# Performance work log

Measured on AMD Instinct MI355X. Metric: run time of the kernel, lower is better.

Reference implementation:

```python
import math
import jax, jax.numpy as jnp
import numpy as np

B, S, E, H = 4, 1024, 768, 12
HD = E // H
NUM_BUCKETS, MAX_DIST = 320, 800


def setup_inputs() -> dict:
    key = jax.random.key(0)
    ks = jax.random.split(key, 8)
    w = lambda k, sh: jax.random.normal(k, sh, jnp.float32) * 0.02
    return {
        "hidden_states": jax.random.normal(ks[0], (B, S, E), jnp.float32),
        "q_w": w(ks[1], (E, E)), "q_b": jnp.zeros((E,), jnp.float32),
        "k_w": w(ks[2], (E, E)), "k_b": jnp.zeros((E,), jnp.float32),
        "v_w": w(ks[3], (E, E)), "v_b": jnp.zeros((E,), jnp.float32),
        "out_w": w(ks[4], (E, E)), "out_b": jnp.zeros((E,), jnp.float32),
        "gru_const": jnp.ones((1, H, 1, 1), jnp.float32),
        "gru_w": w(ks[5], (8, HD)), "gru_b": jnp.zeros((8,), jnp.float32),
        "rel_embed": w(ks[6], (NUM_BUCKETS, H)),
    }


def _relative_positions_bucket(rel):
    # rel: (S, S) int32, rel = memory_pos - context_pos
    nb = NUM_BUCKETS // 2
    buckets = (rel > 0).astype(jnp.int32) * nb
    rel = jnp.abs(rel)
    max_exact = nb // 2
    is_small = rel < max_exact
    large = jnp.log(rel.astype(jnp.float32) / max_exact)
    large = large / math.log(MAX_DIST / max_exact) * (nb - max_exact)
    large = (max_exact + large).astype(jnp.int32)
    large = jnp.minimum(large, nb - 1)
    return buckets + jnp.where(is_small, rel, large)


def _compute_position_bias(rel_embed):
    pos = jnp.arange(S, dtype=jnp.int32)
    rel = pos[None, :] - pos[:, None]              # (S, S)
    bucket = _relative_positions_bucket(rel)       # (S, S) int32
    return rel_embed[bucket].transpose(2, 0, 1)    # (H, S, S)


def reference(hidden_states, q_w, q_b, k_w, k_b, v_w, v_b, out_w, out_b,
              gru_const, gru_w, gru_b, rel_embed):
    position_bias = _compute_position_bias(rel_embed)          # (H, S, S)

    # gated relative-position bias
    ghs = hidden_states.reshape(B, S, H, HD).transpose(0, 2, 1, 3)   # (B,H,S,HD)
    proj = jnp.einsum("bhsd,ed->bhse", ghs, gru_w) + gru_b           # (B,H,S,8)
    proj = proj.reshape(B, H, S, 2, 4).sum(-1)                       # (B,H,S,2)
    gates = jax.nn.sigmoid(proj)
    gate_a, gate_b = gates[..., 0:1], gates[..., 1:2]                # (B,H,S,1)
    gate = gate_a * (gate_b * gru_const - 1.0) + 2.0                 # (B,H,S,1)
    gated_bias = gate[..., None, :, 0][..., None] * 0  # placeholder removed below
    gated_bias = gate * position_bias[None]                          # (B,H,S,S)

    scaling = HD ** -0.5
    q = (hidden_states @ q_w.T + q_b).reshape(B, S, H, HD).transpose(0, 2, 1, 3) * scaling
    k = (hidden_states @ k_w.T + k_b).reshape(B, S, H, HD).transpose(0, 2, 1, 3)
    v = (hidden_states @ v_w.T + v_b).reshape(B, S, H, HD).transpose(0, 2, 1, 3)

    scores = jnp.einsum("bhqd,bhkd->bhqk", q, k) + gated_bias
    attn = jax.nn.softmax(scores, axis=-1)
    ctx = jnp.einsum("bhqk,bhkd->bhqd", attn, v)                     # (B,H,S,HD)
    ctx = ctx.transpose(0, 2, 1, 3).reshape(B, S, E)
    attn_output = ctx @ out_w.T + out_b
    return attn_output, position_bias
```

## Files before the change

### kernel.cpp

```cpp
#include <hip/hip_runtime.h>

typedef unsigned short u16;
typedef __attribute__((ext_vector_type(4))) unsigned short u16x4;
typedef __attribute__((ext_vector_type(8))) short s8v;
typedef __attribute__((ext_vector_type(4))) float f4v;

#define BB 4
#define SS 1024
#define EE 768
#define HH 12
#define DD 64

#define NHS (BB * SS * EE)
#define NW  (EE * EE)
#define LOG2E 1.4426950408889634f

static __device__ __forceinline__ u16 f2bf(float x){
  unsigned int u = __float_as_uint(x);
  u += 0x7fffu + ((u >> 16) & 1u);
  return (u16)(u >> 16);
}
static __device__ __forceinline__ unsigned cvt_pk_bf16(float lo, float hi){
  unsigned r;
  asm("v_cvt_pk_bf16_f32 %0, %1, %2" : "=v"(r) : "v"(lo), "v"(hi));
  return r;
}
static __device__ __forceinline__ void stage16(const u16* g, u16* l){
  __builtin_amdgcn_global_load_lds(
      (const __attribute__((address_space(1))) void*)g,
      (__attribute__((address_space(3))) void*)l, 16, 0, 0);
}

__global__ __launch_bounds__(256) void prep_kernel(const float* __restrict__ hs,
                                                   const float* __restrict__ qw,
                                                   const float* __restrict__ kw,
                                                   const float* __restrict__ vw,
                                                   const float* __restrict__ ow,
                                                   u16* __restrict__ dst,
                                                   const float* __restrict__ rel_embed,
                                                   float* __restrict__ tbl,
                                                   const float* __restrict__ gru_w,
                                                   const float* __restrict__ gru_b,
                                                   const float* __restrict__ gru_c,
                                                   float* __restrict__ gate){
  const int bid = blockIdx.x;
  if (bid < 2688){
    size_t e = ((size_t)bid * 256 + threadIdx.x) * 8;
    const float* src;
    if      (e < (size_t)NHS)            src = hs + e;
    else if (e < (size_t)NHS + NW)       src = qw + (e - NHS);
    else if (e < (size_t)NHS + 2 * NW)   src = kw + (e - NHS - NW);
    else if (e < (size_t)NHS + 3 * NW)   src = vw + (e - NHS - 2 * (size_t)NW);
    else                                 src = ow + (e - NHS - 3 * (size_t)NW);
    f4v v0 = *(const f4v*)src, v1 = *(const f4v*)(src + 4);
    s8v o;
    #pragma unroll
    for (int i = 0; i < 4; i++){ o[i] = (short)f2bf(v0[i]); o[4 + i] = (short)f2bf(v1[i]); }
    size_t row = e / EE;
    int k = (int)(e - row * EE);
    size_t d = row * EE + (size_t)(k ^ (((int)row & 7) << 3));
    *(s8v*)(dst + d) = o;
  } else if (bid < 2784){
    int id = (bid - 2688) * 256 + threadIdx.x;
    int h = id >> 11, r = id & 2047;
    float v = 0.f;
    if (r < 2047){
      int rel = r - 1023;
      int bucket = (rel > 0) ? 160 : 0;
      int a = rel < 0 ? -rel : rel;
      int idx;
      if (a < 80) idx = a;
      else {
        float t = logf((float)a / 80.0f);
        t = t / 2.302585092994046f * 80.0f;
        int lg = (int)(80.0f + t);
        idx = lg < 159 ? lg : 159;
      }
      v = rel_embed[(idx + bucket) * HH + h];
    }
    tbl[id] = v;
  } else {
    int wid = (bid - 2784) * 4 + (threadIdx.x >> 6);
    int lane = threadIdx.x & 63;
    int s = wid & (SS - 1);
    int bh = wid >> 10;
    int h = bh % HH, b = bh / HH;
    float x = hs[(size_t)(b * SS + s) * EE + h * DD + lane];
    float w0 = gru_w[lane] + gru_w[64 + lane] + gru_w[128 + lane] + gru_w[192 + lane];
    float w1 = gru_w[256 + lane] + gru_w[320 + lane] + gru_w[384 + lane] + gru_w[448 + lane];
    float y0 = x * w0, y1 = x * w1;
    #pragma unroll
    for (int off = 1; off < 64; off <<= 1){
      y0 += __shfl_xor(y0, off);
      y1 += __shfl_xor(y1, off);
    }
    if (lane == 0){
      float s0 = y0 + gru_b[0] + gru_b[1] + gru_b[2] + gru_b[3];
      float s1 = y1 + gru_b[4] + gru_b[5] + gru_b[6] + gru_b[7];
      float ga = 1.f / (1.f + __expf(-s0));
      float gb = 1.f / (1.f + __expf(-s1));
      gate[wid] = ga * (gb * gru_c[h] - 1.0f) + 2.0f;
    }
  }
}

template<int EP>
static __device__ __forceinline__ void gemm_body(const u16* __restrict__ A,
                                                 const u16* __restrict__ Bw,
                                                 const float* __restrict__ bias,
                                                 void* __restrict__ Cp,
                                                 float scale, int m0, int n0){
  __shared__ __align__(16) u16 a_s[128 * 64];
  __shared__ __align__(16) u16 b_s[128 * 64];
  const int t = threadIdx.x;
  const int wave = t >> 6, lane = t & 63;
  const int lr = lane & 15, lg = lane >> 4;
  const int wm = (wave >> 1) * 64, wn = (wave & 1) * 64;
  const int srow = lane >> 3;
  const int scol = (lane & 7) * 8;
  const int swz = (lr & 7) << 3;

  const f4v zero = {0.f, 0.f, 0.f, 0.f};
  f4v acc[4][4];
  #pragma unroll
  for (int i = 0; i < 4; i++)
    #pragma unroll
    for (int j = 0; j < 4; j++) acc[i][j] = zero;

  for (int k0 = 0; k0 < EE; k0 += 64){
    if (k0) __syncthreads();
    #pragma unroll
    for (int i = 0; i < 4; i++){
      const int chunk = i * 4 + wave;
      const int r = chunk * 8 + srow;
      stage16(A  + (size_t)(m0 + r) * EE + k0 + scol, &a_s[chunk * 512]);
      stage16(Bw + (size_t)(n0 + r) * EE + k0 + scol, &b_s[chunk * 512]);
    }
    __syncthreads();
    #pragma unroll
    for (int kk = 0; kk < 2; kk++){
      const int cbase = (kk * 32 + lg * 8) ^ swz;
      s8v af[4], bf[4];
      #pragma unroll
      for (int i = 0; i < 4; i++){
        af[i] = *(const s8v*)&a_s[(wm + i * 16 + lr) * 64 + cbase];
        bf[i] = *(const s8v*)&b_s[(wn + i * 16 + lr) * 64 + cbase];
      }
      #pragma unroll
      for (int i = 0; i < 4; i++)
        #pragma unroll
        for (int j = 0; j < 4; j++)
          acc[i][j] = __builtin_amdgcn_mfma_f32_16x16x32_bf16(af[i], bf[j], acc[i][j], 0, 0, 0);
    }
  }

  #pragma unroll
  for (int ii = 0; ii < 4; ii++){
    const int row0 = m0 + wm + ii * 16 + lg * 4;
    const int bb = row0 >> 10;
    const int s0 = row0 & (SS - 1);
    #pragma unroll
    for (int j = 0; j < 4; j++){
      const int col = n0 + wn + j * 16 + lr;
      const float bv = bias[col];
      if (EP == 0){
        const int h = col >> 6, dim = col & 63;
        const int bh = bb * HH + h;
        u16* dst = (u16*)Cp + ((size_t)((bh * 64 + (s0 >> 4)) * 2 + (dim >> 5))) * 512
                   + ((dim >> 3) & 3) * 128 + (s0 & 15) * 8 + (dim & 7);
        #pragma unroll
        for (int r = 0; r < 4; r++)
          dst[r * 8] = f2bf((acc[ii][j][r] + bv) * scale);
      } else if (EP == 2){
        const int h = col >> 6, dim = col & 63;
        const int bh = bb * HH + h;
        u16x4 pk;
        #pragma unroll
        for (int r = 0; r < 4; r++) pk[r] = f2bf(acc[ii][j][r] + bv);
        *(u16x4*)((u16*)Cp + ((size_t)(((bh * 16 + (s0 >> 6)) * 2 + ((s0 >> 5) & 1)) * 4 + (dim >> 4))) * 512
                  + ((s0 >> 3) & 3) * 128 + (dim & 15) * 8 + (s0 & 7)) = pk;
      } else {
        #pragma unroll
        for (int r = 0; r < 4; r++)
          ((float*)Cp)[(size_t)(row0 + r) * EE + col] = acc[ii][j][r] + bv;
      }
    }
  }
}

__global__ __launch_bounds__(256) void gemm_qkv(const u16* __restrict__ A,
                                                const u16* __restrict__ wqkv,
                                                const float* __restrict__ bq,
                                                const float* __restrict__ bk,
                                                const float* __restrict__ bv,
                                                u16* __restrict__ qo,
                                                u16* __restrict__ ko,
                                                u16* __restrict__ vo){
  const int z = blockIdx.z;
  if (z == 2)
    gemm_body<2>(A, wqkv + 2 * (size_t)NW, bv, vo, 1.0f, blockIdx.x * 128, blockIdx.y * 128);
  else
    gemm_body<0>(A, wqkv + (size_t)z * NW, z ? bk : bq, z ? ko : qo,
                 z ? 1.0f : 0.125f * LOG2E, blockIdx.x * 128, blockIdx.y * 128);
}

__global__ __launch_bounds__(256) void gemm_out(const u16* __restrict__ A,
                                                const u16* __restrict__ Bw,
                                                const float* __restrict__ bias,
                                                float* __restrict__ Cp){
  gemm_body<1>(A, Bw, bias, Cp, 1.0f, blockIdx.x * 128, blockIdx.y * 128);
}

__global__ __launch_bounds__(256) void attn_kernel(const u16* __restrict__ qpack,
                                                   const u16* __restrict__ kpack,
                                                   const u16* __restrict__ vpack,
                                                   const float* __restrict__ gate,
                                                   const float* __restrict__ tbl,
                                                   u16* __restrict__ ctx,
                                                   float* __restrict__ pb){
  __shared__ __align__(16) float tbl_s[2048];
  __shared__ __align__(16) u16 p_s[4][16][72];
  const int t = threadIdx.x, wave = t >> 6, lane = t & 63;
  const int lr = lane & 15, lg = lane >> 4;
  const int i = blockIdx.x;
  const int xcd = i & 7, slot = i >> 3;
  const int bhg = xcd * 6 + (slot >> 3);
  const int qb  = slot & 7;
  const int b = bhg / HH, h = bhg % HH;
  const int bh = bhg;
  const int q0w = qb * 128 + wave * 32;
  {
    const float* th = tbl + h * 2048 + t * 8;
    *(f4v*)&tbl_s[t * 8]     = *(const f4v*)th;
    *(f4v*)&tbl_s[t * 8 + 4] = *(const f4v*)(th + 4);
  }
  s8v qf0[2], qf1[2];
  float gt[2];
  #pragma unroll
  for (int g = 0; g < 2; g++){
    const u16* qp = qpack + ((size_t)(bh * 64 + qb * 8 + wave * 2 + g)) * 1024 + lane * 8;
    qf0[g] = *(const s8v*)qp;
    qf1[g] = *(const s8v*)(qp + 512);
    gt[g] = gate[(size_t)bh * SS + q0w + g * 16 + lr] * LOG2E;
  }
  __syncthreads();

  const u16* kp = kpack + (size_t)bh * 65536 + lane * 8;
  const u16* vp = vpack + (size_t)bh * 65536 + lane * 8;

  const f4v zero = {0.f, 0.f, 0.f, 0.f};
  f4v o[2][4];
  float l[2] = {0.f, 0.f};
  #pragma unroll
  for (int g = 0; g < 2; g++)
    #pragma unroll
    for (int d = 0; d < 4; d++) o[g][d] = zero;
  const int voff = lg * 4 - lr;
  const int tb[2] = {1023 - q0w + voff, 1023 - q0w - 16 + voff};
  float* pbh = pb + (size_t)h * (SS * SS);
  const int i0 = (qb * 8 + b * 2) * 16;

  for (int kt = 0; kt < 16; kt++){
    s8v kf0[4], kf1[4];
    #pragma unroll
    for (int n = 0; n < 4; n++){
      const u16* kr = kp + (kt * 4 + n) * 1024;
      kf0[n] = *(const s8v*)kr;
      kf1[n] = *(const s8v*)(kr + 512);
    }
    f4v sf[2][4];
    __builtin_amdgcn_s_setprio(1);
    #pragma unroll
    for (int n = 0; n < 4; n++){
      f4v z0 = zero;
      z0 = __builtin_amdgcn_mfma_f32_16x16x32_bf16(kf0[n], qf0[0], z0, 0, 0, 0);
      z0 = __builtin_amdgcn_mfma_f32_16x16x32_bf16(kf1[n], qf1[0], z0, 0, 0, 0);
      sf[0][n] = z0;
      f4v z1 = zero;
      z1 = __builtin_amdgcn_mfma_f32_16x16x32_bf16(kf0[n], qf0[1], z1, 0, 0, 0);
      z1 = __builtin_amdgcn_mfma_f32_16x16x32_bf16(kf1[n], qf1[1], z1, 0, 0, 0);
      sf[1][n] = z1;
    }
    __builtin_amdgcn_s_setprio(0);
    s8v vf0[4], vf1[4];
    #pragma unroll
    for (int d = 0; d < 4; d++){
      const u16* vr = vp + kt * 4096 + d * 512;
      vf0[d] = *(const s8v*)vr;
      vf1[d] = *(const s8v*)(vr + 2048);
    }
    #pragma unroll
    for (int g = 0; g < 2; g++){
      float ps = 0.f;
      #pragma unroll
      for (int n = 0; n < 4; n++){
        const float* tp = &tbl_s[kt * 64 + n * 16 + tb[g]];
        #pragma unroll
        for (int r = 0; r < 4; r++){
          float p = exp2f(sf[g][n][r] + gt[g] * tp[r]);
          sf[g][n][r] = p;
          ps += p;
        }
      }
      l[g] += ps;
      #pragma unroll
      for (int n = 0; n < 4; n++){
        unsigned pk0 = cvt_pk_bf16(sf[g][n][0], sf[g][n][1]);
        unsigned pk1 = cvt_pk_bf16(sf[g][n][2], sf[g][n][3]);
        u16* prow = &p_s[wave][lr][n * 16 + lg * 4];
        *(unsigned*)prow       = pk0;
        *(unsigned*)(prow + 2) = pk1;
      }
      const s8v pf0 = *(const s8v*)&p_s[wave][lr][lg * 8];
      const s8v pf1 = *(const s8v*)&p_s[wave][lr][32 + lg * 8];
      __builtin_amdgcn_s_setprio(1);
      #pragma unroll
      for (int d = 0; d < 4; d++){
        o[g][d] = __builtin_amdgcn_mfma_f32_16x16x32_bf16(pf0, vf0[d], o[g][d], 0, 0, 0);
        o[g][d] = __builtin_amdgcn_mfma_f32_16x16x32_bf16(pf1, vf1[d], o[g][d], 0, 0, 0);
      }
      __builtin_amdgcn_s_setprio(0);
    }
    {
      #pragma unroll
      for (int rr = 0; rr < 2; rr++){
        const int ii = i0 + kt * 2 + rr;
        const int base = 1023 - ii + t * 4;
        f4v v;
        v[0] = tbl_s[base + 0];
        v[1] = tbl_s[base + 1];
        v[2] = tbl_s[base + 2];
        v[3] = tbl_s[base + 3];
        __builtin_nontemporal_store(v, (f4v*)&pbh[(size_t)ii * SS + t * 4]);
      }
    }
  }
  #pragma unroll
  for (int g = 0; g < 2; g++){
    float lg_ = l[g];
    lg_ += __shfl_xor(lg_, 16);
    lg_ += __shfl_xor(lg_, 32);
    float rl = 1.0f / lg_;
    float linv[4];
    #pragma unroll
    for (int r = 0; r < 4; r++) linv[r] = __shfl(rl, lg * 4 + r);
    #pragma unroll
    for (int d = 0; d < 4; d++)
      #pragma unroll
      for (int r = 0; r < 4; r++){
        float val = o[g][d][r] * linv[r];
        const int row = q0w + g * 16 + lg * 4 + r;
        const int col = (h * DD + d * 16 + lr) ^ ((row & 7) << 3);
        ctx[(size_t)(b * SS + row) * EE + col] = f2bf(val);
      }
  }
}

extern "C" void kernel_launch(void* const* d_in, const int* in_sizes, int n_in,
                              void* d_out, int out_size, void* d_ws, size_t ws_size,
                              hipStream_t stream){
  const float* hs    = (const float*)d_in[0];
  const float* q_w   = (const float*)d_in[1];
  const float* q_b   = (const float*)d_in[2];
  const float* k_w   = (const float*)d_in[3];
  const float* k_b   = (const float*)d_in[4];
  const float* v_w   = (const float*)d_in[5];
  const float* v_b   = (const float*)d_in[6];
  const float* o_w   = (const float*)d_in[7];
  const float* o_b   = (const float*)d_in[8];
  const float* gru_c = (const float*)d_in[9];
  const float* gru_w = (const float*)d_in[10];
  const float* gru_b = (const float*)d_in[11];
  const float* rel   = (const float*)d_in[12];

  float* out0 = (float*)d_out;
  float* pb   = out0 + (size_t)BB * SS * EE;

  char* w = (char*)d_ws;
  u16* qpk  = (u16*)w;  w += (size_t)NHS * 2;
  u16* kpk  = (u16*)w;  w += (size_t)NHS * 2;
  u16* vpk  = (u16*)w;  w += (size_t)NHS * 2;
  u16* cvt  = (u16*)w;  w += ((size_t)NHS + 4 * (size_t)NW) * 2;
  float* gate = (float*)w; w += (size_t)BB * HH * SS * 4;
  float* tbl  = (float*)w;

  u16* hs_bf  = cvt;
  u16* wqkv   = cvt + NHS;
  u16* ow_bf  = cvt + NHS + 3 * (size_t)NW;

  prep_kernel<<<15072, 256, 0, stream>>>(hs, q_w, k_w, v_w, o_w, cvt,
                                         rel, tbl, gru_w, gru_b, gru_c, gate);
  gemm_qkv<<<dim3(32, 6, 3), 256, 0, stream>>>(hs_bf, wqkv, q_b, k_b, v_b, qpk, kpk, vpk);
  attn_kernel<<<384, 256, 0, stream>>>(qpk, kpk, vpk, gate, tbl, hs_bf, pb);
  gemm_out<<<dim3(32, 6), 256, 0, stream>>>(hs_bf, ow_bf, o_b, out0);
}
```

Before: 101.0 us.

## Double-buffer K/V tiles in LDS shared across waves in attention kernel

Each block now stages the K and V tiles for the next key step into a double-buffered shared-memory buffer, and all four waves read their MFMA fragments from it. Before, each wave loaded the same K/V data from global memory on its own. The aim is to cut that redundant global/L2 traffic and overlap the prefetch with compute. In exchange it adds a block-wide barrier every iteration and about 32 KB more LDS per block, which may lower occupancy. The s_setprio hints around the MFMA sections are also removed.

```diff
diff --git a/kernel.cpp b/kernel.cpp
--- a/kernel.cpp
+++ b/kernel.cpp
@@ -219,6 +219,7 @@
                                                    u16* __restrict__ ctx,
                                                    float* __restrict__ pb){
   __shared__ __align__(16) float tbl_s[2048];
+  __shared__ __align__(16) u16 kv_s[2][8192];
   __shared__ __align__(16) u16 p_s[4][16][72];
   const int t = threadIdx.x, wave = t >> 6, lane = t & 63;
   const int lr = lane & 15, lg = lane >> 4;
@@ -243,10 +244,16 @@
     qf1[g] = *(const s8v*)(qp + 512);
     gt[g] = gate[(size_t)bh * SS + q0w + g * 16 + lr] * LOG2E;
   }
+
+  const u16* kbase = kpack + (size_t)bh * 65536;
+  const u16* vbase = vpack + (size_t)bh * 65536;
+  const int so = wave * 1024 + lane * 8;
+
+  stage16(kbase + so,        &kv_s[0][wave * 1024]);
+  stage16(kbase + so + 512,  &kv_s[0][wave * 1024 + 512]);
+  stage16(vbase + so,        &kv_s[0][4096 + wave * 1024]);
+  stage16(vbase + so + 512,  &kv_s[0][4096 + wave * 1024 + 512]);
   __syncthreads();
-
-  const u16* kp = kpack + (size_t)bh * 65536 + lane * 8;
-  const u16* vp = vpack + (size_t)bh * 65536 + lane * 8;
 
   const f4v zero = {0.f, 0.f, 0.f, 0.f};
   f4v o[2][4];
@@ -258,18 +265,29 @@
   const int voff = lg * 4 - lr;
   const int tb[2] = {1023 - q0w + voff, 1023 - q0w - 16 + voff};
   float* pbh = pb + (size_t)h * (SS * SS);
-  const int i0 = (qb * 8 + b * 2) * 16;
+  const int i0 = (qb * 4 + b) * 32;
 
   for (int kt = 0; kt < 16; kt++){
+    const int cur = kt & 1;
+    if (kt < 15){
+      const u16* kg = kbase + (kt + 1) * 4096;
+      const u16* vg = vbase + (kt + 1) * 4096;
+      u16* kl = &kv_s[cur ^ 1][wave * 1024];
+      u16* vl = &kv_s[cur ^ 1][4096 + wave * 1024];
+      stage16(kg + so,       kl);
+      stage16(kg + so + 512, kl + 512);
+      stage16(vg + so,       vl);
+      stage16(vg + so + 512, vl + 512);
+    }
+    const u16* klp = &kv_s[cur][0];
+    const u16* vlp = &kv_s[cur][4096];
     s8v kf0[4], kf1[4];
     #pragma unroll
     for (int n = 0; n < 4; n++){
-      const u16* kr = kp + (kt * 4 + n) * 1024;
-      kf0[n] = *(const s8v*)kr;
-      kf1[n] = *(const s8v*)(kr + 512);
+      kf0[n] = *(const s8v*)&klp[n * 1024 + lane * 8];
+      kf1[n] = *(const s8v*)&klp[n * 1024 + 512 + lane * 8];
     }
     f4v sf[2][4];
-    __builtin_amdgcn_s_setprio(1);
     #pragma unroll
     for (int n = 0; n < 4; n++){
       f4v z0 = zero;
@@ -281,13 +299,11 @@
       z1 = __builtin_amdgcn_mfma_f32_16x16x32_bf16(kf1[n], qf1[1], z1, 0, 0, 0);
       sf[1][n] = z1;
     }
-    __builtin_amdgcn_s_setprio(0);
     s8v vf0[4], vf1[4];
     #pragma unroll
     for (int d = 0; d < 4; d++){
-      const u16* vr = vp + kt * 4096 + d * 512;
-      vf0[d] = *(const s8v*)vr;
-      vf1[d] = *(const s8v*)(vr + 2048);
+      vf0[d] = *(const s8v*)&vlp[d * 512 + lane * 8];
+      vf1[d] = *(const s8v*)&vlp[2048 + d * 512 + lane * 8];
     }
     #pragma unroll
     for (int g = 0; g < 2; g++){
@@ -313,13 +329,11 @@
       }
       const s8v pf0 = *(const s8v*)&p_s[wave][lr][lg * 8];
       const s8v pf1 = *(const s8v*)&p_s[wave][lr][32 + lg * 8];
-      __builtin_amdgcn_s_setprio(1);
       #pragma unroll
       for (int d = 0; d < 4; d++){
         o[g][d] = __builtin_amdgcn_mfma_f32_16x16x32_bf16(pf0, vf0[d], o[g][d], 0, 0, 0);
         o[g][d] = __builtin_amdgcn_mfma_f32_16x16x32_bf16(pf1, vf1[d], o[g][d], 0, 0, 0);
       }
-      __builtin_amdgcn_s_setprio(0);
     }
     {
       #pragma unroll
@@ -334,6 +348,7 @@
         __builtin_nontemporal_store(v, (f4v*)&pbh[(size_t)ii * SS + t * 4]);
       }
     }
+    __syncthreads();
   }
   #pragma unroll
   for (int g = 0; g < 2; g++){
```

New measurement: 105.4 us. 1.04x slower.
